# Optimization experiments

Hardware: AMD Instinct MI355X
Metric: run time of the kernel (lower is better)

Reference implementation:

```python
import jax, jax.numpy as jnp
import numpy as np

N_NODES = 100000
N_EDGES = 3200000
N_FEAT = 512
N_HID = 128
K = 10
ALPHA = 0.1


def setup_inputs() -> dict:
    key = jax.random.key(0)
    k0, k1, k2, k3 = jax.random.split(key, 4)
    x = jax.random.normal(k0, (N_NODES, N_FEAT), dtype=jnp.float32)
    edge_index = jax.random.randint(k1, (2, N_EDGES), 0, N_NODES, dtype=jnp.int32)
    # Linear params (PyTorch default init scale ~ 1/sqrt(fan_in))
    W1 = jax.random.normal(k2, (N_FEAT, N_HID), dtype=jnp.float32) / np.float32(np.sqrt(N_FEAT))
    b1 = jnp.zeros((N_HID,), dtype=jnp.float32)
    W2 = jax.random.normal(k3, (N_HID, N_HID), dtype=jnp.float32) / np.float32(np.sqrt(N_HID))
    b2 = jnp.zeros((N_HID,), dtype=jnp.float32)
    # PPR init of GPR coefficients: temp[k] = alpha*(1-alpha)^k, temp[K] = (1-alpha)^K
    temp = ALPHA * (1.0 - ALPHA) ** np.arange(K + 1)
    temp[-1] = (1.0 - ALPHA) ** K
    temp = jnp.asarray(temp, dtype=jnp.float32)
    return {"x": x, "edge_index": edge_index, "W1": W1, "b1": b1, "W2": W2, "b2": b2, "temp": temp}


def _gcn_norm(edge_index, num_nodes):
    # add self-loops with weight 1, then symmetric normalization D^-1/2 A D^-1/2
    loop = jnp.arange(num_nodes, dtype=edge_index.dtype)
    row = jnp.concatenate([edge_index[0], loop])
    col = jnp.concatenate([edge_index[1], loop])
    w = jnp.ones(row.shape[0], dtype=jnp.float32)
    deg = jax.ops.segment_sum(w, col, num_segments=num_nodes)
    dinv = jnp.where(deg > 0, jax.lax.rsqrt(deg), 0.0)
    norm = dinv[row] * w * dinv[col]
    return row, col, norm


def reference(x, edge_index, W1, b1, W2, b2, temp):
    n = x.shape[0]
    h = jax.nn.relu(x @ W1 + b1)  # lin1 + relu (dropout p=0 is identity)
    h = h @ W2 + b2               # lin2
    row, col, norm = _gcn_norm(edge_index, n)

    def step(carry, gamma):
        hk, acc = carry
        # propagate: gather x_j = hk[row], scale by norm, scatter-add to col
        hk = jax.ops.segment_sum(norm[:, None] * hk[row], col, num_segments=n)
        return (hk, acc + gamma * hk), None

    (_, hidden), _ = jax.lax.scan(step, (h, temp[0] * h), temp[1:])
    return hidden
```

## Files before the change

### kernel.cpp

```cpp
#include <hip/hip_runtime.h>
#include <hip/hip_fp16.h>

#define NN 100000
#define NE 3200000
#define NF 512
#define NH 128
#define NK 10
#define LDA 40
#define SLOT 80

typedef unsigned int u32;
typedef _Float16 f16;
typedef f16 f16x4 __attribute__((ext_vector_type(4)));
typedef f16 f16x8 __attribute__((ext_vector_type(8)));
typedef float f32x4 __attribute__((ext_vector_type(4)));

__device__ __forceinline__ float2 up2(u32 v) {
  __half2 h = *reinterpret_cast<__half2*>(&v);
  return __half22float2(h);
}
__device__ __forceinline__ u32 pk2(float a, float b) {
  __half2 h = __floats2half2_rn(a, b);
  return *reinterpret_cast<u32*>(&h);
}


__global__ void fill_kernel(const int* __restrict__ row, const int* __restrict__ col,
                            int* __restrict__ cnt, int* __restrict__ epack) {
  int chunk = blockIdx.x >> 3;
  int res = blockIdx.x & 7;
  int e = chunk * 256 + threadIdx.x;
  if (e >= NE) return;
  int c = col[e];
  if ((int)((u32)c / 12500u) != res) return;
  int r = row[e];
  int pos = atomicAdd(&cnt[c], 1);
  if (pos < SLOT) epack[c * SLOT + pos] = r;
}

__global__ void dinv_kernel(const int* __restrict__ cnt, float* __restrict__ dinv,
                            float* __restrict__ sdeg) {
  int i = blockIdx.x * 256 + threadIdx.x;
  if (i < NN) {
    float d = (float)(cnt[i] + 1);
    float r = rsqrtf(d);
    dinv[i] = r;
    sdeg[i] = d * r;
  }
}


__global__ __launch_bounds__(256) void gemm1_kernel(
    const float* __restrict__ X, const float* __restrict__ W,
    const float* __restrict__ bias, u32* __restrict__ hout) {
  __shared__ f16 smem[16384];
  __shared__ float bias_s[NH];
  f16* As = smem;
  f16* Bs = smem + 128 * LDA;
  int tid = threadIdx.x;
  int wave = tid >> 6, lane = tid & 63;
  int quad = lane >> 4, l16 = lane & 15;
  int row0 = blockIdx.x * 128;
  if (tid < NH) bias_s[tid] = bias[tid];

  f32x4 acc[2][8];
#pragma unroll
  for (int t = 0; t < 2; ++t)
#pragma unroll
    for (int u = 0; u < 8; ++u) acc[t][u] = (f32x4){0.f, 0.f, 0.f, 0.f};

  for (int k0 = 0; k0 < NF; k0 += 32) {
#pragma unroll
    for (int i = 0; i < 4; ++i) {
      int slot = tid + i * 256;
      int r = slot >> 3, q4 = slot & 7;
      int grow = row0 + r;
      float4 v = make_float4(0.f, 0.f, 0.f, 0.f);
      if (grow < NN) v = *(const float4*)(X + (size_t)grow * NF + k0 + q4 * 4);
      f16x4 h;
      h[0] = (f16)v.x; h[1] = (f16)v.y; h[2] = (f16)v.z; h[3] = (f16)v.w;
      *(f16x4*)(As + r * LDA + q4 * 4) = h;
    }
#pragma unroll
    for (int i = 0; i < 4; ++i) {
      int slot = tid + i * 256;
      int n = slot & 127, k4 = slot >> 7;
      f16x4 h;
#pragma unroll
      for (int j = 0; j < 4; ++j) h[j] = (f16)W[(size_t)(k0 + k4 * 4 + j) * NH + n];
      *(f16x4*)(Bs + n * LDA + k4 * 4) = h;
    }
    __syncthreads();
    f16x8 a0 = *(f16x8*)(As + (wave * 32 + l16) * LDA + quad * 8);
    f16x8 a1 = *(f16x8*)(As + (wave * 32 + 16 + l16) * LDA + quad * 8);
#pragma unroll
    for (int u = 0; u < 8; ++u) {
      f16x8 b = *(f16x8*)(Bs + (u * 16 + l16) * LDA + quad * 8);
      acc[0][u] = __builtin_amdgcn_mfma_f32_16x16x32_f16(a0, b, acc[0][u], 0, 0, 0);
      acc[1][u] = __builtin_amdgcn_mfma_f32_16x16x32_f16(a1, b, acc[1][u], 0, 0, 0);
    }
    __syncthreads();
  }
#pragma unroll
  for (int t = 0; t < 2; ++t)
#pragma unroll
    for (int u = 0; u < 8; ++u)
#pragma unroll
      for (int r = 0; r < 4; ++r) {
        int row = wave * 32 + t * 16 + quad * 4 + r;
        int col = u * 16 + l16;
        float v = acc[t][u][r] + bias_s[col];
        smem[row * 128 + col] = (f16)fmaxf(v, 0.f);
      }
  __syncthreads();
  const u32* os = (const u32*)smem;
#pragma unroll
  for (int i = 0; i < 8; ++i) {
    int idx4 = tid + i * 256;
    int row = idx4 >> 4;
    int grow = row0 + row;
    if (grow < NN) {
      uint4 v = *(const uint4*)(os + idx4 * 4);
      *(uint4*)(hout + (size_t)grow * 64 + (idx4 * 4 & 63)) = v;
    }
  }
}

__global__ __launch_bounds__(256) void gemm2_kernel(
    const u32* __restrict__ Xh, const float* __restrict__ W,
    const float* __restrict__ bias, const float* __restrict__ dinv,
    u32* __restrict__ hout) {
  __shared__ f16 smem[16384];
  __shared__ float bias_s[NH];
  __shared__ float dinv_s[128];
  f16* As = smem;
  f16* Bs = smem + 128 * LDA;
  int tid = threadIdx.x;
  int wave = tid >> 6, lane = tid & 63;
  int quad = lane >> 4, l16 = lane & 15;
  int row0 = blockIdx.x * 128;
  if (tid < NH) bias_s[tid] = bias[tid];
  if (tid < 128) {
    int grow = row0 + tid;
    dinv_s[tid] = (grow < NN) ? dinv[grow] : 1.0f;
  }

  f32x4 acc[2][8];
#pragma unroll
  for (int t = 0; t < 2; ++t)
#pragma unroll
    for (int u = 0; u < 8; ++u) acc[t][u] = (f32x4){0.f, 0.f, 0.f, 0.f};

  for (int k0 = 0; k0 < NH; k0 += 32) {
#pragma unroll
    for (int i = 0; i < 2; ++i) {
      int slot = tid + i * 256;
      int r = slot >> 2, q = slot & 3;
      int grow = row0 + r;
      uint4 v = make_uint4(0, 0, 0, 0);
      if (grow < NN) v = *(const uint4*)(Xh + (size_t)grow * 64 + (k0 >> 1) + q * 4);
      *(uint4*)(As + r * LDA + q * 8) = v;
    }
#pragma unroll
    for (int i = 0; i < 4; ++i) {
      int slot = tid + i * 256;
      int n = slot & 127, k4 = slot >> 7;
      f16x4 h;
#pragma unroll
      for (int j = 0; j < 4; ++j) h[j] = (f16)W[(size_t)(k0 + k4 * 4 + j) * NH + n];
      *(f16x4*)(Bs + n * LDA + k4 * 4) = h;
    }
    __syncthreads();
    f16x8 a0 = *(f16x8*)(As + (wave * 32 + l16) * LDA + quad * 8);
    f16x8 a1 = *(f16x8*)(As + (wave * 32 + 16 + l16) * LDA + quad * 8);
#pragma unroll
    for (int u = 0; u < 8; ++u) {
      f16x8 b = *(f16x8*)(Bs + (u * 16 + l16) * LDA + quad * 8);
      acc[0][u] = __builtin_amdgcn_mfma_f32_16x16x32_f16(a0, b, acc[0][u], 0, 0, 0);
      acc[1][u] = __builtin_amdgcn_mfma_f32_16x16x32_f16(a1, b, acc[1][u], 0, 0, 0);
    }
    __syncthreads();
  }
#pragma unroll
  for (int t = 0; t < 2; ++t)
#pragma unroll
    for (int u = 0; u < 8; ++u)
#pragma unroll
      for (int r = 0; r < 4; ++r) {
        int row = wave * 32 + t * 16 + quad * 4 + r;
        int col = u * 16 + l16;
        smem[row * 128 + col] = (f16)((acc[t][u][r] + bias_s[col]) * dinv_s[row]);
      }
  __syncthreads();
  const u32* os = (const u32*)smem;
#pragma unroll
  for (int i = 0; i < 8; ++i) {
    int idx4 = tid + i * 256;
    int row = idx4 >> 4;
    int grow = row0 + row;
    if (grow < NN) {
      uint4 v = *(const uint4*)(os + idx4 * 4);
      *(uint4*)(hout + (size_t)grow * 64 + (idx4 * 4 & 63)) = v;
    }
  }
}


#define ACC8(v)                                          \
  {                                                      \
    float2 f_;                                           \
    f_ = up2((v).x); acc[0] += f_.x; acc[1] += f_.y;     \
    f_ = up2((v).y); acc[2] += f_.x; acc[3] += f_.y;     \
    f_ = up2((v).z); acc[4] += f_.x; acc[5] += f_.y;     \
    f_ = up2((v).w); acc[6] += f_.x; acc[7] += f_.y;     \
  }

__global__ __launch_bounds__(256) void prop_kernel(
    const u32* __restrict__ src, u32* __restrict__ dst,
    const float* __restrict__ dinv, const int* __restrict__ cnt,
    const int* __restrict__ epack) {
  int wave = threadIdx.x >> 6;
  int lane = threadIdx.x & 63;
  int g = lane >> 4;
  int l = lane & 15;
  int node = blockIdx.x * 4 + wave;
  if (node >= NN) return;
  int deg = cnt[node];
  if (deg > SLOT) deg = SLOT;
  int beg = node * SLOT;
  int end = beg + deg;
  const uint4* s4 = (const uint4*)src;
  float acc[8];
#pragma unroll
  for (int i = 0; i < 8; ++i) acc[i] = 0.f;

  for (int base = beg; base < end; base += 64) {
    int idx = base + lane;
    int r = 0;
    if (idx < end) {
      r = epack[idx];
      r = (r < 0) ? 0 : ((r >= NN) ? NN - 1 : r);
    }
    int m = end - base;
    if (m > 64) m = 64;
    int full = m >> 2;
    int j = 0;
    for (; j + 4 <= full; j += 4) {
      int r0 = __shfl(r, j * 4 + g);
      int r1 = __shfl(r, j * 4 + 4 + g);
      int r2 = __shfl(r, j * 4 + 8 + g);
      int r3 = __shfl(r, j * 4 + 12 + g);
      uint4 v0 = s4[(size_t)r0 * 16 + l];
      uint4 v1 = s4[(size_t)r1 * 16 + l];
      uint4 v2 = s4[(size_t)r2 * 16 + l];
      uint4 v3 = s4[(size_t)r3 * 16 + l];
      ACC8(v0);
      ACC8(v1);
      ACC8(v2);
      ACC8(v3);
    }
    for (; j < full; ++j) {
      int rj = __shfl(r, j * 4 + g);
      uint4 v = s4[(size_t)rj * 16 + l];
      ACC8(v);
    }
    int rem = m & 3;
    if (rem) {
      int rj = __shfl(r, full * 4 + g);
      if (g < rem) {
        uint4 v = s4[(size_t)rj * 16 + l];
        ACC8(v);
      }
    }
  }
  if (g == 0) {
    uint4 v = s4[(size_t)node * 16 + l];
    ACC8(v);
  }
#pragma unroll
  for (int i = 0; i < 8; ++i) {
    acc[i] += __shfl_xor(acc[i], 16);
    acc[i] += __shfl_xor(acc[i], 32);
  }
  if (g == 0) {
    float di = dinv[node];
    float ds = di * di;
    uint4 o;
    o.x = pk2(ds * acc[0], ds * acc[1]);
    o.y = pk2(ds * acc[2], ds * acc[3]);
    o.z = pk2(ds * acc[4], ds * acc[5]);
    o.w = pk2(ds * acc[6], ds * acc[7]);
    ((uint4*)dst)[(size_t)node * 16 + l] = o;
  }
}


__global__ void sum6_kernel(const u32* __restrict__ b0, const u32* __restrict__ b1,
                            const u32* __restrict__ b2, const u32* __restrict__ b3,
                            const u32* __restrict__ b4, const u32* __restrict__ b5,
                            const float* __restrict__ sdeg,
                            const float* __restrict__ temp, float* __restrict__ out) {
  int i = blockIdx.x * 256 + threadIdx.x;
  float sd = sdeg[i >> 6];
  float2 s = make_float2(0.f, 0.f);
  float2 v;
  v = up2(b0[i]); s.x = fmaf(temp[0], v.x, s.x); s.y = fmaf(temp[0], v.y, s.y);
  v = up2(b1[i]); s.x = fmaf(temp[1], v.x, s.x); s.y = fmaf(temp[1], v.y, s.y);
  v = up2(b2[i]); s.x = fmaf(temp[2], v.x, s.x); s.y = fmaf(temp[2], v.y, s.y);
  v = up2(b3[i]); s.x = fmaf(temp[3], v.x, s.x); s.y = fmaf(temp[3], v.y, s.y);
  v = up2(b4[i]); s.x = fmaf(temp[4], v.x, s.x); s.y = fmaf(temp[4], v.y, s.y);
  v = up2(b5[i]); s.x = fmaf(temp[5], v.x, s.x); s.y = fmaf(temp[5], v.y, s.y);
  float2 o;
  o.x = sd * s.x;
  o.y = sd * s.y;
  ((float2*)out)[i] = o;
}

__global__ void sum5_kernel(const u32* __restrict__ b0, const u32* __restrict__ b1,
                            const u32* __restrict__ b2, const u32* __restrict__ b3,
                            const u32* __restrict__ b4,
                            const float* __restrict__ sdeg,
                            const float* __restrict__ temp, float* __restrict__ out) {
  int i = blockIdx.x * 256 + threadIdx.x;
  float sd = sdeg[i >> 6];
  float2 t = make_float2(0.f, 0.f);
  float2 v;
  v = up2(b0[i]); t.x = fmaf(temp[6], v.x, t.x); t.y = fmaf(temp[6], v.y, t.y);
  v = up2(b1[i]); t.x = fmaf(temp[7], v.x, t.x); t.y = fmaf(temp[7], v.y, t.y);
  v = up2(b2[i]); t.x = fmaf(temp[8], v.x, t.x); t.y = fmaf(temp[8], v.y, t.y);
  v = up2(b3[i]); t.x = fmaf(temp[9], v.x, t.x); t.y = fmaf(temp[9], v.y, t.y);
  v = up2(b4[i]); t.x = fmaf(temp[10], v.x, t.x); t.y = fmaf(temp[10], v.y, t.y);
  float2 s = ((float2*)out)[i];
  s.x = fmaf(sd, t.x, s.x);
  s.y = fmaf(sd, t.y, s.y);
  ((float2*)out)[i] = s;
}


extern "C" void kernel_launch(void* const* d_in, const int* in_sizes, int n_in,
                              void* d_out, int out_size, void* d_ws, size_t ws_size,
                              hipStream_t stream) {
  const float* x = (const float*)d_in[0];
  const int* erow_in = (const int*)d_in[1];
  const int* ecol_in = erow_in + NE;
  const float* W1 = (const float*)d_in[2];
  const float* b1 = (const float*)d_in[3];
  const float* W2 = (const float*)d_in[4];
  const float* b2 = (const float*)d_in[5];
  const float* temp = (const float*)d_in[6];

  char* w = (char*)d_ws;
  size_t o = 0;
  auto alloc = [&](size_t bytes) -> void* {
    void* p = w + o;
    o += (bytes + 255) & ~(size_t)255;
    return p;
  };
  int* cnt = (int*)alloc((size_t)NN * 4);
  float* dinv = (float*)alloc((size_t)NN * 4);
  float* sdeg = (float*)alloc((size_t)NN * 4);
  int* epack = (int*)alloc((size_t)NN * SLOT * 4);
  u32* bufA = (u32*)alloc((size_t)NN * 64 * 4);
  u32* B[5];
  for (int i = 0; i < 5; ++i) B[i] = (u32*)alloc((size_t)NN * 64 * 4);
  float* outp = (float*)d_out;
  (void)ws_size;

  hipMemsetAsync(cnt, 0, (size_t)NN * 4, stream);
  fill_kernel<<<(NE / 256) * 8, 256, 0, stream>>>(erow_in, ecol_in, cnt, epack);
  dinv_kernel<<<(NN + 255) / 256, 256, 0, stream>>>(cnt, dinv, sdeg);

  int gblocks = (NN + 127) / 128;
  gemm1_kernel<<<gblocks, 256, 0, stream>>>(x, W1, b1, bufA);
  gemm2_kernel<<<gblocks, 256, 0, stream>>>(bufA, W2, b2, dinv, B[0]);

  int pblocks = (NN + 3) / 4;
  prop_kernel<<<pblocks, 256, 0, stream>>>(B[0], B[1], dinv, cnt, epack);
  prop_kernel<<<pblocks, 256, 0, stream>>>(B[1], B[2], dinv, cnt, epack);
  prop_kernel<<<pblocks, 256, 0, stream>>>(B[2], B[3], dinv, cnt, epack);
  prop_kernel<<<pblocks, 256, 0, stream>>>(B[3], B[4], dinv, cnt, epack);
  prop_kernel<<<pblocks, 256, 0, stream>>>(B[4], bufA, dinv, cnt, epack);
  sum6_kernel<<<NN * 64 / 256, 256, 0, stream>>>(B[0], B[1], B[2], B[3], B[4], bufA,
                                                 sdeg, temp, outp);
  prop_kernel<<<pblocks, 256, 0, stream>>>(bufA, B[0], dinv, cnt, epack);
  prop_kernel<<<pblocks, 256, 0, stream>>>(B[0], B[1], dinv, cnt, epack);
  prop_kernel<<<pblocks, 256, 0, stream>>>(B[1], B[2], dinv, cnt, epack);
  prop_kernel<<<pblocks, 256, 0, stream>>>(B[2], B[3], dinv, cnt, epack);
  prop_kernel<<<pblocks, 256, 0, stream>>>(B[3], B[4], dinv, cnt, epack);
  sum5_kernel<<<NN * 64 / 256, 256, 0, stream>>>(B[0], B[1], B[2], B[3], B[4], sdeg,
                                                 temp, outp);
}
```

Before: 1.661 ms.

## Build compact CSR and split features into 8 column slabs for propagation

Replaces the padded 80-slot-per-node edge buckets with a compacted CSR built by a prefix scan plus compaction pass. The hidden feature buffers are reorganized into 8 slabs of 16 features each, and each propagation block works on one slab. The intent is that one slab's gather working set (about 3.2MB) stays cache-resident, and that the index stream shrinks. In exchange it adds several preprocessing kernels, reads the edge indices 8 times per propagation step, and narrows gathers to 32-bit loads per lane with more per-node loop overhead.

```diff
diff --git a/kernel.cpp b/kernel.cpp
--- a/kernel.cpp
+++ b/kernel.cpp
@@ -8,6 +8,8 @@
 #define NK 10
 #define LDA 40
 #define SLOT 80
+#define SL (NN * 8)
+#define NB 3125
 
 typedef unsigned int u32;
 typedef _Float16 f16;
@@ -25,17 +27,20 @@
 }
 
 
-__global__ void fill_kernel(const int* __restrict__ row, const int* __restrict__ col,
-                            int* __restrict__ cnt, int* __restrict__ epack) {
-  int chunk = blockIdx.x >> 3;
+__global__ __launch_bounds__(256) void fill_kernel(const int* __restrict__ row,
+                                                   const int* __restrict__ col,
+                                                   int* __restrict__ cnt,
+                                                   int* __restrict__ bucket) {
   int res = blockIdx.x & 7;
-  int e = chunk * 256 + threadIdx.x;
-  if (e >= NE) return;
-  int c = col[e];
-  if ((int)((u32)c / 12500u) != res) return;
-  int r = row[e];
-  int pos = atomicAdd(&cnt[c], 1);
-  if (pos < SLOT) epack[c * SLOT + pos] = r;
+  for (int chunk = blockIdx.x >> 3; chunk < NE / 256; chunk += 256) {
+    int e = chunk * 256 + threadIdx.x;
+    int c = col[e];
+    if ((int)((u32)c / 12500u) == res) {
+      int r = row[e];
+      int pos = atomicAdd(&cnt[c], 1);
+      if (pos < SLOT) bucket[c * SLOT + pos] = r;
+    }
+  }
 }
 
 __global__ void dinv_kernel(const int* __restrict__ cnt, float* __restrict__ dinv,
@@ -47,6 +52,81 @@
     dinv[i] = r;
     sdeg[i] = d * r;
   }
+}
+
+
+__global__ __launch_bounds__(256) void bsum_kernel(const int* __restrict__ cnt,
+                                                   int* __restrict__ bsum) {
+  int b = blockIdx.x;
+  int t = threadIdx.x;
+  int base = b * 1024;
+  int s = 0;
+#pragma unroll
+  for (int j = 0; j < 4; ++j) {
+    int i = base + t + j * 256;
+    if (i < NN) {
+      int v = cnt[i];
+      if (v > SLOT) v = SLOT;
+      s += v;
+    }
+  }
+  for (int off = 32; off > 0; off >>= 1) s += __shfl_down(s, off);
+  __shared__ int wsum[4];
+  if ((t & 63) == 0) wsum[t >> 6] = s;
+  __syncthreads();
+  if (t == 0) bsum[b] = wsum[0] + wsum[1] + wsum[2] + wsum[3];
+}
+
+__global__ void scan98_kernel(const int* __restrict__ bsum, int* __restrict__ boff,
+                              int* __restrict__ colptr) {
+  __shared__ int buf[128];
+  int t = threadIdx.x;
+  int v = (t < 98) ? bsum[t] : 0;
+  buf[t] = v;
+  __syncthreads();
+  for (int off = 1; off < 128; off <<= 1) {
+    int a = (t >= off) ? buf[t - off] : 0;
+    __syncthreads();
+    buf[t] += a;
+    __syncthreads();
+  }
+  if (t < 98) boff[t] = buf[t] - v;
+  if (t == 97) colptr[NN] = buf[t];
+}
+
+__global__ __launch_bounds__(1024) void localscan_kernel(const int* __restrict__ cnt,
+                                                         const int* __restrict__ boff,
+                                                         int* __restrict__ colptr) {
+  __shared__ int buf[1024];
+  int b = blockIdx.x;
+  int t = threadIdx.x;
+  int i = b * 1024 + t;
+  int v = 0;
+  if (i < NN) {
+    v = cnt[i];
+    if (v > SLOT) v = SLOT;
+  }
+  buf[t] = v;
+  __syncthreads();
+  for (int off = 1; off < 1024; off <<= 1) {
+    int a = (t >= off) ? buf[t - off] : 0;
+    __syncthreads();
+    buf[t] += a;
+    __syncthreads();
+  }
+  if (i < NN) colptr[i] = boff[b] + buf[t] - v;
+}
+
+__global__ void compact_kernel(const int* __restrict__ cnt,
+                               const int* __restrict__ colptr,
+                               const int* __restrict__ bucket,
+                               int* __restrict__ dense) {
+  int s = blockIdx.x * 256 + threadIdx.x;
+  int node = (int)((u32)s / (u32)SLOT);
+  int pos = s - node * SLOT;
+  int deg = cnt[node];
+  if (deg > SLOT) deg = SLOT;
+  if (pos < deg) dense[colptr[node] + pos] = bucket[s];
 }
 
 
@@ -193,104 +273,91 @@
       }
   __syncthreads();
   const u32* os = (const u32*)smem;
+  int r = tid >> 1, half = tid & 1;
+  int grow = row0 + r;
 #pragma unroll
   for (int i = 0; i < 8; ++i) {
-    int idx4 = tid + i * 256;
-    int row = idx4 >> 4;
-    int grow = row0 + row;
     if (grow < NN) {
-      uint4 v = *(const uint4*)(os + idx4 * 4);
-      *(uint4*)(hout + (size_t)grow * 64 + (idx4 * 4 & 63)) = v;
-    }
-  }
-}
-
-
-#define ACC8(v)                                          \
-  {                                                      \
-    float2 f_;                                           \
-    f_ = up2((v).x); acc[0] += f_.x; acc[1] += f_.y;     \
-    f_ = up2((v).y); acc[2] += f_.x; acc[3] += f_.y;     \
-    f_ = up2((v).z); acc[4] += f_.x; acc[5] += f_.y;     \
-    f_ = up2((v).w); acc[6] += f_.x; acc[7] += f_.y;     \
-  }
+      uint4 v = *(const uint4*)(os + r * 64 + i * 8 + half * 4);
+      *(uint4*)(hout + (size_t)i * SL + (size_t)grow * 8 + half * 4) = v;
+    }
+  }
+}
+
 
 __global__ __launch_bounds__(256) void prop_kernel(
     const u32* __restrict__ src, u32* __restrict__ dst,
-    const float* __restrict__ dinv, const int* __restrict__ cnt,
-    const int* __restrict__ epack) {
+    const float* __restrict__ dinv, const int* __restrict__ colptr,
+    const int* __restrict__ eidx) {
+  int c = blockIdx.x / NB;
+  int nb = blockIdx.x - c * NB;
   int wave = threadIdx.x >> 6;
   int lane = threadIdx.x & 63;
-  int g = lane >> 4;
-  int l = lane & 15;
-  int node = blockIdx.x * 4 + wave;
-  if (node >= NN) return;
-  int deg = cnt[node];
-  if (deg > SLOT) deg = SLOT;
-  int beg = node * SLOT;
-  int end = beg + deg;
-  const uint4* s4 = (const uint4*)src;
-  float acc[8];
-#pragma unroll
-  for (int i = 0; i < 8; ++i) acc[i] = 0.f;
-
-  for (int base = beg; base < end; base += 64) {
-    int idx = base + lane;
-    int r = 0;
-    if (idx < end) {
-      r = epack[idx];
-      r = (r < 0) ? 0 : ((r >= NN) ? NN - 1 : r);
-    }
-    int m = end - base;
-    if (m > 64) m = 64;
-    int full = m >> 2;
-    int j = 0;
-    for (; j + 4 <= full; j += 4) {
-      int r0 = __shfl(r, j * 4 + g);
-      int r1 = __shfl(r, j * 4 + 4 + g);
-      int r2 = __shfl(r, j * 4 + 8 + g);
-      int r3 = __shfl(r, j * 4 + 12 + g);
-      uint4 v0 = s4[(size_t)r0 * 16 + l];
-      uint4 v1 = s4[(size_t)r1 * 16 + l];
-      uint4 v2 = s4[(size_t)r2 * 16 + l];
-      uint4 v3 = s4[(size_t)r3 * 16 + l];
-      ACC8(v0);
-      ACC8(v1);
-      ACC8(v2);
-      ACC8(v3);
-    }
-    for (; j < full; ++j) {
-      int rj = __shfl(r, j * 4 + g);
-      uint4 v = s4[(size_t)rj * 16 + l];
-      ACC8(v);
-    }
-    int rem = m & 3;
-    if (rem) {
-      int rj = __shfl(r, full * 4 + g);
-      if (g < rem) {
-        uint4 v = s4[(size_t)rj * 16 + l];
-        ACC8(v);
-      }
-    }
-  }
-  if (g == 0) {
-    uint4 v = s4[(size_t)node * 16 + l];
-    ACC8(v);
-  }
-#pragma unroll
-  for (int i = 0; i < 8; ++i) {
-    acc[i] += __shfl_xor(acc[i], 16);
-    acc[i] += __shfl_xor(acc[i], 32);
-  }
-  if (g == 0) {
-    float di = dinv[node];
-    float ds = di * di;
-    uint4 o;
-    o.x = pk2(ds * acc[0], ds * acc[1]);
-    o.y = pk2(ds * acc[2], ds * acc[3]);
-    o.z = pk2(ds * acc[4], ds * acc[5]);
-    o.w = pk2(ds * acc[6], ds * acc[7]);
-    ((uint4*)dst)[(size_t)node * 16 + l] = o;
+  int g = lane >> 3;
+  int l = lane & 7;
+  const u32* s = src + (size_t)c * SL;
+  u32* d = dst + (size_t)c * SL;
+  int node0 = nb * 32 + wave * 8;
+  for (int ni = 0; ni < 8; ++ni) {
+    int node = node0 + ni;
+    int beg = colptr[node];
+    int deg = colptr[node + 1] - beg;
+    float a0 = 0.f, a1 = 0.f;
+    for (int base = 0; base < deg; base += 64) {
+      int idx = base + lane;
+      int r = 0;
+      if (idx < deg) {
+        r = eidx[beg + idx];
+        r = (r < 0) ? 0 : ((r >= NN) ? NN - 1 : r);
+      }
+      int m = deg - base;
+      if (m > 64) m = 64;
+      int full = m >> 3;
+      int j = 0;
+      for (; j + 4 <= full; j += 4) {
+        int r0 = __shfl(r, j * 8 + g);
+        int r1 = __shfl(r, j * 8 + 8 + g);
+        int r2 = __shfl(r, j * 8 + 16 + g);
+        int r3 = __shfl(r, j * 8 + 24 + g);
+        u32 v0 = s[(size_t)r0 * 8 + l];
+        u32 v1 = s[(size_t)r1 * 8 + l];
+        u32 v2 = s[(size_t)r2 * 8 + l];
+        u32 v3 = s[(size_t)r3 * 8 + l];
+        float2 f;
+        f = up2(v0); a0 += f.x; a1 += f.y;
+        f = up2(v1); a0 += f.x; a1 += f.y;
+        f = up2(v2); a0 += f.x; a1 += f.y;
+        f = up2(v3); a0 += f.x; a1 += f.y;
+      }
+      for (; j < full; ++j) {
+        int rj = __shfl(r, j * 8 + g);
+        u32 v = s[(size_t)rj * 8 + l];
+        float2 f = up2(v);
+        a0 += f.x; a1 += f.y;
+      }
+      int rem = m & 7;
+      if (rem) {
+        int rj = __shfl(r, full * 8 + g);
+        if (g < rem) {
+          u32 v = s[(size_t)rj * 8 + l];
+          float2 f = up2(v);
+          a0 += f.x; a1 += f.y;
+        }
+      }
+    }
+    if (g == 0) {
+      u32 v = s[(size_t)node * 8 + l];
+      float2 f = up2(v);
+      a0 += f.x; a1 += f.y;
+    }
+    a0 += __shfl_xor(a0, 8);  a1 += __shfl_xor(a1, 8);
+    a0 += __shfl_xor(a0, 16); a1 += __shfl_xor(a1, 16);
+    a0 += __shfl_xor(a0, 32); a1 += __shfl_xor(a1, 32);
+    if (g == 0) {
+      float di = dinv[node];
+      float ds = di * di;
+      d[(size_t)node * 8 + l] = pk2(ds * a0, ds * a1);
+    }
   }
 }
 
@@ -300,8 +367,11 @@
                             const u32* __restrict__ b4, const u32* __restrict__ b5,
                             const float* __restrict__ sdeg,
                             const float* __restrict__ temp, float* __restrict__ out) {
-  int i = blockIdx.x * 256 + threadIdx.x;
-  float sd = sdeg[i >> 6];
+  int pos = blockIdx.x * 256 + threadIdx.x;
+  size_t i = (size_t)blockIdx.y * SL + pos;
+  int node = pos >> 3;
+  int within = pos & 7;
+  float sd = sdeg[node];
   float2 s = make_float2(0.f, 0.f);
   float2 v;
   v = up2(b0[i]); s.x = fmaf(temp[0], v.x, s.x); s.y = fmaf(temp[0], v.y, s.y);
@@ -313,7 +383,7 @@
   float2 o;
   o.x = sd * s.x;
   o.y = sd * s.y;
-  ((float2*)out)[i] = o;
+  ((float2*)out)[(size_t)node * 64 + blockIdx.y * 8 + within] = o;
 }
 
 __global__ void sum5_kernel(const u32* __restrict__ b0, const u32* __restrict__ b1,
@@ -321,8 +391,11 @@
                             const u32* __restrict__ b4,
                             const float* __restrict__ sdeg,
                             const float* __restrict__ temp, float* __restrict__ out) {
-  int i = blockIdx.x * 256 + threadIdx.x;
-  float sd = sdeg[i >> 6];
+  int pos = blockIdx.x * 256 + threadIdx.x;
+  size_t i = (size_t)blockIdx.y * SL + pos;
+  int node = pos >> 3;
+  int within = pos & 7;
+  float sd = sdeg[node];
   float2 t = make_float2(0.f, 0.f);
   float2 v;
   v = up2(b0[i]); t.x = fmaf(temp[6], v.x, t.x); t.y = fmaf(temp[6], v.y, t.y);
@@ -330,10 +403,11 @@
   v = up2(b2[i]); t.x = fmaf(temp[8], v.x, t.x); t.y = fmaf(temp[8], v.y, t.y);
   v = up2(b3[i]); t.x = fmaf(temp[9], v.x, t.x); t.y = fmaf(temp[9], v.y, t.y);
   v = up2(b4[i]); t.x = fmaf(temp[10], v.x, t.x); t.y = fmaf(temp[10], v.y, t.y);
-  float2 s = ((float2*)out)[i];
+  size_t oi = (size_t)node * 64 + blockIdx.y * 8 + within;
+  float2 s = ((float2*)out)[oi];
   s.x = fmaf(sd, t.x, s.x);
   s.y = fmaf(sd, t.y, s.y);
-  ((float2*)out)[i] = s;
+  ((float2*)out)[oi] = s;
 }
 
 
@@ -359,34 +433,42 @@
   int* cnt = (int*)alloc((size_t)NN * 4);
   float* dinv = (float*)alloc((size_t)NN * 4);
   float* sdeg = (float*)alloc((size_t)NN * 4);
-  int* epack = (int*)alloc((size_t)NN * SLOT * 4);
+  int* colptr = (int*)alloc((size_t)(NN + 1) * 4);
+  int* bsum = (int*)alloc(128 * 4);
+  int* boff = (int*)alloc(128 * 4);
+  int* dense = (int*)alloc((size_t)NE * 4);
   u32* bufA = (u32*)alloc((size_t)NN * 64 * 4);
   u32* B[5];
   for (int i = 0; i < 5; ++i) B[i] = (u32*)alloc((size_t)NN * 64 * 4);
+  int* bucket = (int*)bufA;
   float* outp = (float*)d_out;
   (void)ws_size;
 
   hipMemsetAsync(cnt, 0, (size_t)NN * 4, stream);
-  fill_kernel<<<(NE / 256) * 8, 256, 0, stream>>>(erow_in, ecol_in, cnt, epack);
+  fill_kernel<<<2048, 256, 0, stream>>>(erow_in, ecol_in, cnt, bucket);
   dinv_kernel<<<(NN + 255) / 256, 256, 0, stream>>>(cnt, dinv, sdeg);
+  bsum_kernel<<<98, 256, 0, stream>>>(cnt, bsum);
+  scan98_kernel<<<1, 128, 0, stream>>>(bsum, boff, colptr);
+  localscan_kernel<<<98, 1024, 0, stream>>>(cnt, boff, colptr);
+  compact_kernel<<<NN * SLOT / 256, 256, 0, stream>>>(cnt, colptr, bucket, dense);
 
   int gblocks = (NN + 127) / 128;
   gemm1_kernel<<<gblocks, 256, 0, stream>>>(x, W1, b1, bufA);
   gemm2_kernel<<<gblocks, 256, 0, stream>>>(bufA, W2, b2, dinv, B[0]);
 
-  int pblocks = (NN + 3) / 4;
-  prop_kernel<<<pblocks, 256, 0, stream>>>(B[0], B[1], dinv, cnt, epack);
-  prop_kernel<<<pblocks, 256, 0, stream>>>(B[1], B[2], dinv, cnt, epack);
-  prop_kernel<<<pblocks, 256, 0, stream>>>(B[2], B[3], dinv, cnt, epack);
-  prop_kernel<<<pblocks, 256, 0, stream>>>(B[3], B[4], dinv, cnt, epack);
-  prop_kernel<<<pblocks, 256, 0, stream>>>(B[4], bufA, dinv, cnt, epack);
-  sum6_kernel<<<NN * 64 / 256, 256, 0, stream>>>(B[0], B[1], B[2], B[3], B[4], bufA,
-                                                 sdeg, temp, outp);
-  prop_kernel<<<pblocks, 256, 0, stream>>>(bufA, B[0], dinv, cnt, epack);
-  prop_kernel<<<pblocks, 256, 0, stream>>>(B[0], B[1], dinv, cnt, epack);
-  prop_kernel<<<pblocks, 256, 0, stream>>>(B[1], B[2], dinv, cnt, epack);
-  prop_kernel<<<pblocks, 256, 0, stream>>>(B[2], B[3], dinv, cnt, epack);
-  prop_kernel<<<pblocks, 256, 0, stream>>>(B[3], B[4], dinv, cnt, epack);
-  sum5_kernel<<<NN * 64 / 256, 256, 0, stream>>>(B[0], B[1], B[2], B[3], B[4], sdeg,
-                                                 temp, outp);
-}
+  dim3 sgrid(SL / 256, 8);
+  prop_kernel<<<NB * 8, 256, 0, stream>>>(B[0], B[1], dinv, colptr, dense);
+  prop_kernel<<<NB * 8, 256, 0, stream>>>(B[1], B[2], dinv, colptr, dense);
+  prop_kernel<<<NB * 8, 256, 0, stream>>>(B[2], B[3], dinv, colptr, dense);
+  prop_kernel<<<NB * 8, 256, 0, stream>>>(B[3], B[4], dinv, colptr, dense);
+  prop_kernel<<<NB * 8, 256, 0, stream>>>(B[4], bufA, dinv, colptr, dense);
+  sum6_kernel<<<sgrid, 256, 0, stream>>>(B[0], B[1], B[2], B[3], B[4], bufA, sdeg,
+                                         temp, outp);
+  prop_kernel<<<NB * 8, 256, 0, stream>>>(bufA, B[0], dinv, colptr, dense);
+  prop_kernel<<<NB * 8, 256, 0, stream>>>(B[0], B[1], dinv, colptr, dense);
+  prop_kernel<<<NB * 8, 256, 0, stream>>>(B[1], B[2], dinv, colptr, dense);
+  prop_kernel<<<NB * 8, 256, 0, stream>>>(B[2], B[3], dinv, colptr, dense);
+  prop_kernel<<<NB * 8, 256, 0, stream>>>(B[3], B[4], dinv, colptr, dense);
+  sum5_kernel<<<sgrid, 256, 0, stream>>>(B[0], B[1], B[2], B[3], B[4], sdeg, temp,
+                                         outp);
+}
```

Measured after the change: 3.299 ms. +98.6%, slower.
